# Kernel tuning notes

Measured on AMD Instinct MI355X. Metric: run time of the kernel, lower is better.

Reference implementation:

```python
import jax, jax.numpy as jnp
import numpy as np

B, N, D, K, L, H, DFF = 2048, 64, 256, 32, 2, 8, 1024
TEMP = 10.0
EPS = 1e-10


def _ln(x, g, b):
    m = jnp.mean(x, -1, keepdims=True)
    v = jnp.mean((x - m) ** 2, -1, keepdims=True)
    return (x - m) * jax.lax.rsqrt(v + 1e-5) * g + b


def _mha(x, Wqkv, bqkv, Wo, bo):
    b, n, d = x.shape
    dh = d // H
    qkv = x @ Wqkv.T + bqkv                      # [b,n,3d]
    q, k, v = jnp.split(qkv, 3, axis=-1)
    q = q.reshape(b, n, H, dh)
    k = k.reshape(b, n, H, dh)
    v = v.reshape(b, n, H, dh)
    att = jnp.einsum('bqhd,bkhd->bhqk', q, k) / np.float32(np.sqrt(dh))
    att = jax.nn.softmax(att, axis=-1)
    o = jnp.einsum('bhqk,bkhd->bqhd', att, v).reshape(b, n, d)
    return o @ Wo.T + bo


def _encoder(x, Wqkv, bqkv, Wo, bo, ln1_g, ln1_b, ln2_g, ln2_b, W1, b1, W2, b2):
    # torch TransformerEncoder, norm_first=False (post-LN), dropout=0
    for l in range(L):
        x = _ln(x + _mha(x, Wqkv[l], bqkv[l], Wo[l], bo[l]), ln1_g[l], ln1_b[l])
        h = jax.nn.relu(x @ W1[l].T + b1[l]) @ W2[l].T + b2[l]
        x = _ln(x + h, ln2_g[l], ln2_b[l])
    return x


def _cluster_probs_from_emb(emb, mus):
    # ||x - tanh(mu)||^2 via expansion to avoid the [B,N,K,D] intermediate
    mt = jnp.tanh(mus)                                       # [K,D]
    d2 = (jnp.sum(emb ** 2, -1)[..., None]
          - 2.0 * jnp.einsum('bnd,kd->bnk', emb, mt)
          + jnp.sum(mt ** 2, -1))                            # [B,N,K]
    e = jnp.exp(-d2 / TEMP)
    return e / jnp.sum(e, -1, keepdims=True)


def _forward(input_series, init_logits, transition_logits,
             Wqkv, bqkv, Wo, bo, ln1_g, ln1_b, ln2_g, ln2_b,
             W1, b1, W2, b2, mus):
    prob_pi = jax.nn.softmax(init_logits, axis=0)            # [K]
    prob_A = jax.nn.softmax(transition_logits, axis=1)       # [K,K]
    emb_all = _encoder(input_series, Wqkv, bqkv, Wo, bo,
                       ln1_g, ln1_b, ln2_g, ln2_b, W1, b1, W2, b2)
    logits_all = _cluster_probs_from_emb(emb_all, mus)       # [B,N,K]

    log_emit = jnp.log(logits_all + EPS)                     # [B,N,K]
    lt0 = jax.nn.softmax(jnp.log(prob_pi + EPS)[None, :] + log_emit[:, 0], axis=1)

    def step(lt, le):
        lt = jax.nn.softmax(jnp.log(lt @ prob_A + EPS) + le, axis=1)
        return lt, lt

    _, rest = jax.lax.scan(step, lt0, jnp.swapaxes(log_emit[:, 1:], 0, 1))
    cluster_probs = jnp.concatenate([lt0[:, None], jnp.swapaxes(rest, 0, 1)], axis=1)
    entropy_loss = -jnp.mean(jnp.sum(cluster_probs * jnp.log(cluster_probs + EPS), -1))
    return cluster_probs, emb_all, prob_pi, prob_A, entropy_loss


def setup_inputs() -> dict:
    key = jax.random.key(0)
    ks = jax.random.split(key, 10)
    s = jnp.float32(0.02)
    return {
        'input_series': jax.random.normal(ks[0], (B, N, D), jnp.float32),
        'init_logits': jax.random.normal(ks[1], (K,), jnp.float32),
        'transition_logits': jax.random.normal(ks[2], (K, K), jnp.float32),
        'Wqkv': jax.random.normal(ks[3], (L, 3 * D, D), jnp.float32) * s,
        'bqkv': jnp.zeros((L, 3 * D), jnp.float32),
        'Wo': jax.random.normal(ks[4], (L, D, D), jnp.float32) * s,
        'bo': jnp.zeros((L, D), jnp.float32),
        'ln1_g': jnp.ones((L, D), jnp.float32),
        'ln1_b': jnp.zeros((L, D), jnp.float32),
        'ln2_g': jnp.ones((L, D), jnp.float32),
        'ln2_b': jnp.zeros((L, D), jnp.float32),
        'W1': jax.random.normal(ks[5], (L, DFF, D), jnp.float32) * s,
        'b1': jnp.zeros((L, DFF), jnp.float32),
        'W2': jax.random.normal(ks[6], (L, D, DFF), jnp.float32) * s,
        'b2': jnp.zeros((L, D), jnp.float32),
        'mus': jax.random.normal(ks[7], (K, D), jnp.float32),
    }


def reference(input_series, init_logits, transition_logits, Wqkv, bqkv, Wo, bo,
              ln1_g, ln1_b, ln2_g, ln2_b, W1, b1, W2, b2, mus):
    return _forward(input_series, init_logits, transition_logits, Wqkv, bqkv,
                    Wo, bo, ln1_g, ln1_b, ln2_g, ln2_b, W1, b1, W2, b2, mus)
```

## Files before the change

kernel.cpp:

```cpp
#include <hip/hip_runtime.h>

#define BB   2048
#define NNX  64
#define DD   256
#define KKC  32
#define LLN  2
#define HHN  8
#define DHH  32
#define DFFN 1024
#define BNT  (BB*NNX)

typedef short s16x8 __attribute__((ext_vector_type(8)));
typedef float f32x4 __attribute__((ext_vector_type(4)));

#define GLOAD_LDS16(gp, lp) __builtin_amdgcn_global_load_lds( \
    (const __attribute__((address_space(1))) void*)(gp),      \
    (__attribute__((address_space(3))) void*)(lp), 16, 0, 0)

#define WAITVM4() asm volatile("s_waitcnt vmcnt(4)" ::: "memory")
#define WAITVM0() asm volatile("s_waitcnt vmcnt(0)" ::: "memory")
#define SBAR() __builtin_amdgcn_s_barrier()

__device__ __forceinline__ unsigned short f2bf(float f) {
  unsigned int u = __float_as_uint(f);
  u += 0x7fffu + ((u >> 16) & 1u);
  return (unsigned short)(u >> 16);
}
__device__ __forceinline__ float bf2f(unsigned short u) {
  return __uint_as_float(((unsigned int)u) << 16);
}

__global__ __launch_bounds__(256) void cvt_kernel(const float4* __restrict__ src,
                                                  ushort4* __restrict__ dst, int n4) {
  int i = blockIdx.x * 256 + threadIdx.x;
  int st = gridDim.x * 256;
  for (; i < n4; i += st) {
    float4 v = src[i];
    ushort4 o;
    o.x = f2bf(v.x); o.y = f2bf(v.y); o.z = f2bf(v.z); o.w = f2bf(v.w);
    dst[i] = o;
  }
}

__global__ void mt_kernel(const float* __restrict__ mus, float* __restrict__ mtT,
                          float* __restrict__ mtn) {
  int k = threadIdx.x;
  if (k < 32) {
    float acc = 0.f;
    for (int d = 0; d < 256; d++) {
      float t = tanhf(mus[k * 256 + d]);
      mtT[d * 32 + k] = t;
      acc += t * t;
    }
    mtn[k] = acc;
  }
}

__global__ void piA_kernel(const float* __restrict__ il, const float* __restrict__ tl,
                           float* __restrict__ d_pi, float* __restrict__ d_A,
                           float* __restrict__ d_ent) {
  int lane = threadIdx.x;
  if (lane == 0) *d_ent = 0.f;
  if (lane < 32) {
    float v = il[lane];
    float mx = v;
    #pragma unroll
    for (int off = 16; off; off >>= 1) mx = fmaxf(mx, __shfl_xor(mx, off, 32));
    float e = expf(v - mx), sm = e;
    #pragma unroll
    for (int off = 16; off; off >>= 1) sm += __shfl_xor(sm, off, 32);
    d_pi[lane] = e / sm;
    for (int r = 0; r < 32; r++) {
      float a = tl[r * 32 + lane];
      float m2 = a;
      #pragma unroll
      for (int off = 16; off; off >>= 1) m2 = fmaxf(m2, __shfl_xor(m2, off, 32));
      float e2 = expf(a - m2), s2 = e2;
      #pragma unroll
      for (int off = 16; off; off >>= 1) s2 += __shfl_xor(s2, off, 32);
      d_A[r * 32 + lane] = e2 / s2;
    }
  }
}

template <int EPI>
__global__ __launch_bounds__(256, 4) void gemm_nt(const unsigned short* __restrict__ A,
                                                  const unsigned short* __restrict__ Bw,
                                                  const float* __restrict__ bias,
                                                  unsigned short* __restrict__ outp,
                                                  int N, int K, int nx) {
  __shared__ unsigned short lds[16384];
  const int t = threadIdx.x;
  const int bid = blockIdx.x, nwg = gridDim.x;
  const int wg = (bid & 7) * (nwg >> 3) + (bid >> 3);
  const int m0 = (wg / nx) << 7;
  const int n0 = (wg % nx) << 7;
  const int lane = t & 63, w = t >> 6;
  const int wm = w >> 1, wn = w & 1;
  const int lr = lane & 15, lk = lane >> 4;

  const int r0 = t >> 2, sg = t & 3;
  const int s0 = sg ^ ((r0 >> 1) & 3);
  const int r1 = r0 + 64;
  const int s1 = sg ^ ((r1 >> 1) & 3);
  const int aoff0 = (m0 + r0) * K + s0 * 8;
  const int aoff1 = (m0 + r1) * K + s1 * 8;
  const int boff0 = (n0 + r0) * K + s0 * 8;
  const int boff1 = (n0 + r1) * K + s1 * 8;

#define STAGE(buf, k0) do {                                    \
    char* la = (char*)lds + (buf) * 16384;                     \
    GLOAD_LDS16(A + aoff0 + (k0), la + t * 16);                \
    GLOAD_LDS16(A + aoff1 + (k0), la + 4096 + t * 16);         \
    GLOAD_LDS16(Bw + boff0 + (k0), la + 8192 + t * 16);        \
    GLOAD_LDS16(Bw + boff1 + (k0), la + 12288 + t * 16);       \
  } while (0)

  f32x4 acc[4][4];
  #pragma unroll
  for (int i = 0; i < 4; i++)
    #pragma unroll
    for (int j = 0; j < 4; j++) acc[i][j] = (f32x4)(0.f);

  const int ra = wm * 64 + lr, rb = wn * 64 + lr;
  const int sla = lk ^ ((ra >> 1) & 3), slb = lk ^ ((rb >> 1) & 3);

  const int NT = K >> 5;
  STAGE(0, 0);
  STAGE(1, 32);
  WAITVM4();
  SBAR();

  int c = 0;
  for (int kt = 0; kt < NT; kt++) {
    s16x8 af[4], bf[4];
    {
      const unsigned short* ua = lds + c * 8192;
      const unsigned short* ub = ua + 4096;
      #pragma unroll
      for (int mf = 0; mf < 4; mf++)
        af[mf] = *(const s16x8*)&ua[(ra + mf * 16) * 32 + sla * 8];
      #pragma unroll
      for (int nf = 0; nf < 4; nf++)
        bf[nf] = *(const s16x8*)&ub[(rb + nf * 16) * 32 + slb * 8];
    }
    __builtin_amdgcn_s_setprio(1);
    #pragma unroll
    for (int mf = 0; mf < 4; mf++)
      #pragma unroll
      for (int nf = 0; nf < 4; nf++)
        acc[mf][nf] = __builtin_amdgcn_mfma_f32_16x16x32_bf16(af[mf], bf[nf], acc[mf][nf], 0, 0, 0);
    __builtin_amdgcn_s_setprio(0);
    SBAR();
    if (kt < NT - 2) {
      STAGE(c, (kt + 2) << 5);
      WAITVM4();
    } else if (kt == NT - 2) {
      WAITVM0();
    }
    SBAR();
    c ^= 1;
  }
#undef STAGE

  #pragma unroll
  for (int nf = 0; nf < 4; nf++) {
    int col = n0 + wn * 64 + nf * 16 + lr;
    float bv = bias[col];
    #pragma unroll
    for (int mf = 0; mf < 4; mf++)
      #pragma unroll
      for (int r = 0; r < 4; r++) {
        int row = m0 + wm * 64 + mf * 16 + lk * 4 + r;
        float v = acc[mf][nf][r] + bv;
        if (EPI == 1) v = fmaxf(v, 0.f);
        outp[(size_t)row * N + col] = f2bf(v);
      }
  }
}

template <bool WR32>
__global__ __launch_bounds__(512) void gemm_ln(const unsigned short* __restrict__ A,
                                               const unsigned short* __restrict__ Bw,
                                               const float* __restrict__ bias,
                                               const unsigned short* __restrict__ res,
                                               const float* __restrict__ g,
                                               const float* __restrict__ bta,
                                               unsigned short* __restrict__ xb,
                                               float* __restrict__ x32,
                                               int K) {
  __shared__ unsigned short As[128 * 64];
  __shared__ unsigned short Bs[256 * 64];
  __shared__ float stats[2][128][4];
  const int t = threadIdx.x;
  const int nwg = gridDim.x;
  const int bid = blockIdx.x;
  const int wg = (bid & 7) * (nwg >> 3) + (bid >> 3);
  const int m0 = wg << 7;

  const int lane = t & 63, w = t >> 6;
  const int wm = w >> 2, wn = w & 3;
  const int lr = lane & 15, lk = lane >> 4;

  size_t aoff[2], boff[4];
  #pragma unroll
  for (int p = 0; p < 2; p++) {
    int u = p * 512 + t;
    int row = u >> 3, sp = u & 7;
    int seg = sp ^ (((row >> 2) & 1) << 1);
    aoff[p] = (size_t)(m0 + row) * K + seg * 8;
  }
  #pragma unroll
  for (int p = 0; p < 4; p++) {
    int u = p * 512 + t;
    int row = u >> 3, sp = u & 7;
    int seg = sp ^ (((row >> 2) & 1) << 1);
    boff[p] = (size_t)row * K + seg * 8;
  }

  f32x4 acc[4][4];
  #pragma unroll
  for (int i = 0; i < 4; i++)
    #pragma unroll
    for (int j = 0; j < 4; j++) acc[i][j] = (f32x4)(0.f);

  for (int k0 = 0; k0 < K; k0 += 64) {
    #pragma unroll
    for (int p = 0; p < 2; p++)
      GLOAD_LDS16(A + aoff[p] + k0, (char*)As + (p * 512 + t) * 16);
    #pragma unroll
    for (int p = 0; p < 4; p++)
      GLOAD_LDS16(Bw + boff[p] + k0, (char*)Bs + (p * 512 + t) * 16);
    __syncthreads();
    #pragma unroll
    for (int z = 0; z < 2; z++) {
      s16x8 af[4], bfr[4];
      #pragma unroll
      for (int mf = 0; mf < 4; mf++) {
        int row = wm * 64 + mf * 16 + lr;
        int cc = (z * 4 + lk) ^ (((row >> 2) & 1) << 1);
        af[mf] = *(const s16x8*)&As[row * 64 + cc * 8];
      }
      #pragma unroll
      for (int nf = 0; nf < 4; nf++) {
        int row = wn * 64 + nf * 16 + lr;
        int cc = (z * 4 + lk) ^ (((row >> 2) & 1) << 1);
        bfr[nf] = *(const s16x8*)&Bs[row * 64 + cc * 8];
      }
      #pragma unroll
      for (int mf = 0; mf < 4; mf++)
        #pragma unroll
        for (int nf = 0; nf < 4; nf++)
          acc[mf][nf] = __builtin_amdgcn_mfma_f32_16x16x32_bf16(af[mf], bfr[nf], acc[mf][nf], 0, 0, 0);
    }
    __syncthreads();
  }

  float bv[4];
  #pragma unroll
  for (int nf = 0; nf < 4; nf++) bv[nf] = bias[wn * 64 + nf * 16 + lr];

  #pragma unroll
  for (int mf = 0; mf < 4; mf++) {
    #pragma unroll
    for (int r = 0; r < 4; r++) {
      int grow = m0 + wm * 64 + mf * 16 + lk * 4 + r;
      float s = 0.f, q = 0.f;
      #pragma unroll
      for (int nf = 0; nf < 4; nf++) {
        int col = wn * 64 + nf * 16 + lr;
        float v = acc[mf][nf][r] + bv[nf] + bf2f(res[(size_t)grow * 256 + col]);
        acc[mf][nf][r] = v;
        s += v; q += v * v;
      }
      #pragma unroll
      for (int off = 1; off < 16; off <<= 1) { s += __shfl_xor(s, off); q += __shfl_xor(q, off); }
      if (lr == 0) {
        int lrow = wm * 64 + mf * 16 + lk * 4 + r;
        stats[0][lrow][wn] = s;
        stats[1][lrow][wn] = q;
      }
    }
  }
  __syncthreads();

  float gv[4], bbv[4];
  #pragma unroll
  for (int nf = 0; nf < 4; nf++) {
    int col = wn * 64 + nf * 16 + lr;
    gv[nf] = g[col]; bbv[nf] = bta[col];
  }
  #pragma unroll
  for (int mf = 0; mf < 4; mf++) {
    #pragma unroll
    for (int r = 0; r < 4; r++) {
      int lrow = wm * 64 + mf * 16 + lk * 4 + r;
      int grow = m0 + lrow;
      float s4 = stats[0][lrow][0] + stats[0][lrow][1] + stats[0][lrow][2] + stats[0][lrow][3];
      float q4 = stats[1][lrow][0] + stats[1][lrow][1] + stats[1][lrow][2] + stats[1][lrow][3];
      float mean = s4 * (1.f / 256.f);
      float var = q4 * (1.f / 256.f) - mean * mean;
      float rs = rsqrtf(var + 1e-5f);
      #pragma unroll
      for (int nf = 0; nf < 4; nf++) {
        int col = wn * 64 + nf * 16 + lr;
        float val = (acc[mf][nf][r] - mean) * rs * gv[nf] + bbv[nf];
        xb[(size_t)grow * 256 + col] = f2bf(val);
        if (WR32) x32[(size_t)grow * 256 + col] = val;
      }
    }
  }
}

__global__ __launch_bounds__(64) void attn_kernel(const unsigned short* __restrict__ qkv,
                                                  unsigned short* __restrict__ ob) {
  __shared__ unsigned short qs[64 * 32], ks[64 * 32], vs[64 * 32];
  __shared__ unsigned short ps[64 * 72];
  const int bh = blockIdx.x;
  const int b = bh >> 3, h = bh & 7;
  const int lane = threadIdx.x;
  const int lr = lane & 15, lk = lane >> 4;

  #pragma unroll
  for (int p = 0; p < 4; p++) {
    int u = lane + p * 64;
    int row = u >> 2, seg = u & 3;
    size_t gb = (size_t)(b * 64 + row) * 768 + h * 32 + seg * 8;
    GLOAD_LDS16(qkv + gb, (char*)qs + u * 16);
    GLOAD_LDS16(qkv + gb + 256, (char*)ks + u * 16);
    GLOAD_LDS16(qkv + gb + 512, (char*)vs + u * 16);
  }
  __syncthreads();

  f32x4 s[4][4];
  #pragma unroll
  for (int i = 0; i < 4; i++)
    #pragma unroll
    for (int j = 0; j < 4; j++) s[i][j] = (f32x4)(0.f);
  s16x8 aq[4], bk[4];
  #pragma unroll
  for (int mi = 0; mi < 4; mi++) aq[mi] = *(const s16x8*)&qs[(mi * 16 + lr) * 32 + lk * 8];
  #pragma unroll
  for (int nj = 0; nj < 4; nj++) bk[nj] = *(const s16x8*)&ks[(nj * 16 + lr) * 32 + lk * 8];
  #pragma unroll
  for (int mi = 0; mi < 4; mi++)
    #pragma unroll
    for (int nj = 0; nj < 4; nj++)
      s[mi][nj] = __builtin_amdgcn_mfma_f32_16x16x32_bf16(aq[mi], bk[nj], s[mi][nj], 0, 0, 0);

  const float scale = 0.17677669529663687f;
  #pragma unroll
  for (int mi = 0; mi < 4; mi++) {
    #pragma unroll
    for (int r = 0; r < 4; r++) {
      float t0 = s[mi][0][r] * scale, t1 = s[mi][1][r] * scale;
      float t2 = s[mi][2][r] * scale, t3 = s[mi][3][r] * scale;
      float mx = fmaxf(fmaxf(t0, t1), fmaxf(t2, t3));
      #pragma unroll
      for (int off = 8; off; off >>= 1) mx = fmaxf(mx, __shfl_xor(mx, off, 16));
      float e0 = expf(t0 - mx), e1 = expf(t1 - mx), e2 = expf(t2 - mx), e3 = expf(t3 - mx);
      float sm = e0 + e1 + e2 + e3;
      #pragma unroll
      for (int off = 8; off; off >>= 1) sm += __shfl_xor(sm, off, 16);
      float inv = 1.f / sm;
      int prow = mi * 16 + lk * 4 + r;
      ps[prow * 72 + lr + 0]  = f2bf(e0 * inv);
      ps[prow * 72 + lr + 16] = f2bf(e1 * inv);
      ps[prow * 72 + lr + 32] = f2bf(e2 * inv);
      ps[prow * 72 + lr + 48] = f2bf(e3 * inv);
    }
  }
  __syncthreads();

  f32x4 oacc[4][2];
  #pragma unroll
  for (int i = 0; i < 4; i++) { oacc[i][0] = (f32x4)(0.f); oacc[i][1] = (f32x4)(0.f); }
  #pragma unroll
  for (int kk = 0; kk < 2; kk++) {
    s16x8 bv[2];
    #pragma unroll
    for (int nf = 0; nf < 2; nf++) {
      s16x8 tmp;
      #pragma unroll
      for (int jj = 0; jj < 8; jj++)
        tmp[jj] = (short)vs[(kk * 32 + lk * 8 + jj) * 32 + nf * 16 + lr];
      bv[nf] = tmp;
    }
    #pragma unroll
    for (int mi = 0; mi < 4; mi++) {
      s16x8 ap = *(const s16x8*)&ps[(mi * 16 + lr) * 72 + kk * 32 + lk * 8];
      #pragma unroll
      for (int nf = 0; nf < 2; nf++)
        oacc[mi][nf] = __builtin_amdgcn_mfma_f32_16x16x32_bf16(ap, bv[nf], oacc[mi][nf], 0, 0, 0);
    }
  }
  #pragma unroll
  for (int mi = 0; mi < 4; mi++)
    #pragma unroll
    for (int nf = 0; nf < 2; nf++)
      #pragma unroll
      for (int r = 0; r < 4; r++) {
        int tok = mi * 16 + lk * 4 + r;
        int c = nf * 16 + lr;
        ob[(size_t)(b * 64 + tok) * 256 + h * 32 + c] = f2bf(oacc[mi][nf][r]);
      }
}

__global__ __launch_bounds__(256) void cluster_kernel(const float* __restrict__ x,
                                                      const float* __restrict__ mtT,
                                                      const float* __restrict__ mtn,
                                                      float* __restrict__ log_emit) {
  __shared__ float mts[8192];
  __shared__ float es[4][256];
  const int t = threadIdx.x;
  #pragma unroll
  for (int i = 0; i < 8; i++)
    ((float4*)mts)[i * 256 + t] = ((const float4*)mtT)[i * 256 + t];
  const int w = t >> 6, lane = t & 63;
  const int k = lane & 31, half = lane >> 5;
  const float mtnr = mtn[k];
  __syncthreads();
  #pragma unroll 1
  for (int it = 0; it < 8; it++) {
    size_t tok = (size_t)blockIdx.x * 32 + (size_t)w * 8 + it;
    float4 u = *((const float4*)(x + tok * 256) + lane);
    *(float4*)&es[w][lane * 4] = u;
    float e2 = u.x * u.x + u.y * u.y + u.z * u.z + u.w * u.w;
    #pragma unroll
    for (int off = 1; off < 64; off <<= 1) e2 += __shfl_xor(e2, off);
    float acc = 0.f;
    const float* ep = &es[w][half * 128];
    const float* mp = &mts[half * 128 * 32 + k];
    #pragma unroll
    for (int d = 0; d < 128; d += 4) {
      float4 ev = *(const float4*)(ep + d);
      acc += ev.x * mp[(d + 0) * 32] + ev.y * mp[(d + 1) * 32]
           + ev.z * mp[(d + 2) * 32] + ev.w * mp[(d + 3) * 32];
    }
    acc += __shfl_xor(acc, 32);
    float d2 = e2 - 2.f * acc + mtnr;
    float e = expf(-d2 * 0.1f);
    float sm = e;
    #pragma unroll
    for (int off = 16; off; off >>= 1) sm += __shfl_xor(sm, off, 32);
    if (half == 0) log_emit[tok * 32 + k] = logf(e / sm + 1e-10f);
  }
}

__global__ __launch_bounds__(256) void scan_kernel(const float* __restrict__ log_emit,
                                                   const float* __restrict__ pi,
                                                   const float* __restrict__ A,
                                                   float* __restrict__ cp,
                                                   float* __restrict__ ent) {
  const int g = threadIdx.x >> 5, j = threadIdx.x & 31;
  const int batch = blockIdx.x * 8 + g;
  float regA[32];
  #pragma unroll
  for (int i = 0; i < 32; i++) regA[i] = A[i * 32 + j];
  const float* le = log_emit + (size_t)batch * 64 * 32;
  float* cpo = cp + (size_t)batch * 64 * 32;

  float u = logf(pi[j] + 1e-10f) + le[j];
  float mx = u;
  #pragma unroll
  for (int off = 16; off; off >>= 1) mx = fmaxf(mx, __shfl_xor(mx, off, 32));
  float e = expf(u - mx), sm = e;
  #pragma unroll
  for (int off = 16; off; off >>= 1) sm += __shfl_xor(sm, off, 32);
  float p = e / sm;
  cpo[j] = p;
  float enta = p * logf(p + 1e-10f);

  for (int n = 1; n < 64; n++) {
    float tt = 0.f;
    #pragma unroll
    for (int i = 0; i < 32; i++) tt += __shfl(p, i, 32) * regA[i];
    u = logf(tt + 1e-10f) + le[n * 32 + j];
    mx = u;
    #pragma unroll
    for (int off = 16; off; off >>= 1) mx = fmaxf(mx, __shfl_xor(mx, off, 32));
    e = expf(u - mx); sm = e;
    #pragma unroll
    for (int off = 16; off; off >>= 1) sm += __shfl_xor(sm, off, 32);
    p = e / sm;
    cpo[n * 32 + j] = p;
    enta += p * logf(p + 1e-10f);
  }
  #pragma unroll
  for (int off = 16; off; off >>= 1) enta += __shfl_xor(enta, off, 32);
  if (j == 0) atomicAdd(ent, -enta * (1.f / (2048.f * 64.f)));
}

extern "C" void kernel_launch(void* const* d_in, const int* in_sizes, int n_in,
                              void* d_out, int out_size, void* d_ws, size_t ws_size,
                              hipStream_t stream) {
  const float* input = (const float*)d_in[0];
  const float* init_logits = (const float*)d_in[1];
  const float* trans = (const float*)d_in[2];
  const float* Wqkv = (const float*)d_in[3];
  const float* bqkv = (const float*)d_in[4];
  const float* Wo = (const float*)d_in[5];
  const float* bo = (const float*)d_in[6];
  const float* ln1g = (const float*)d_in[7];
  const float* ln1b = (const float*)d_in[8];
  const float* ln2g = (const float*)d_in[9];
  const float* ln2b = (const float*)d_in[10];
  const float* W1 = (const float*)d_in[11];
  const float* b1 = (const float*)d_in[12];
  const float* W2 = (const float*)d_in[13];
  const float* b2 = (const float*)d_in[14];
  const float* mus = (const float*)d_in[15];

  float* out = (float*)d_out;
  float* cp = out;
  float* x = out + 4194304;
  float* d_pi = out + 37748736;
  float* d_A = out + 37748768;
  float* d_ent = out + 37749792;

  char* ws = (char*)d_ws;
  unsigned short* qkv = (unsigned short*)ws;
  unsigned short* hb = (unsigned short*)ws;
  float* log_emit = (float*)ws;
  unsigned short* ob = (unsigned short*)(ws + 268435456ull);
  unsigned short* xb = (unsigned short*)(ws + 335544320ull);
  unsigned short* wq_b = (unsigned short*)(ws + 402653184ull);
  unsigned short* wo_b = (unsigned short*)(ws + 402653184ull + 786432ull);
  unsigned short* w1_b = (unsigned short*)(ws + 402653184ull + 1048576ull);
  unsigned short* w2_b = (unsigned short*)(ws + 402653184ull + 2097152ull);
  float* mtT = (float*)(ws + 402653184ull + 3145728ull);
  float* mtn = (float*)(ws + 402653184ull + 3178496ull);

  cvt_kernel<<<2048, 256, 0, stream>>>((const float4*)input, (ushort4*)xb, BNT * 256 / 4);
  cvt_kernel<<<256, 256, 0, stream>>>((const float4*)Wqkv, (ushort4*)wq_b, LLN * 768 * 256 / 4);
  cvt_kernel<<<256, 256, 0, stream>>>((const float4*)Wo, (ushort4*)wo_b, LLN * 256 * 256 / 4);
  cvt_kernel<<<256, 256, 0, stream>>>((const float4*)W1, (ushort4*)w1_b, LLN * 1024 * 256 / 4);
  cvt_kernel<<<256, 256, 0, stream>>>((const float4*)W2, (ushort4*)w2_b, LLN * 256 * 1024 / 4);
  mt_kernel<<<1, 64, 0, stream>>>(mus, mtT, mtn);
  piA_kernel<<<1, 64, 0, stream>>>(init_logits, trans, d_pi, d_A, d_ent);

  for (int l = 0; l < 2; l++) {
    gemm_nt<0><<<6144, 256, 0, stream>>>(xb, wq_b + l * 196608, bqkv + l * 768,
                                         qkv, 768, 256, 6);
    attn_kernel<<<16384, 64, 0, stream>>>(qkv, ob);
    gemm_ln<false><<<1024, 512, 0, stream>>>(ob, wo_b + l * 65536, bo + l * 256,
                                             xb, ln1g + l * 256, ln1b + l * 256,
                                             xb, nullptr, 256);
    gemm_nt<1><<<8192, 256, 0, stream>>>(xb, w1_b + l * 262144, b1 + l * 1024,
                                         hb, 1024, 256, 8);
    if (l == LLN - 1)
      gemm_ln<true><<<1024, 512, 0, stream>>>(hb, w2_b + l * 262144, b2 + l * 256,
                                              xb, ln2g + l * 256, ln2b + l * 256,
                                              xb, x, 1024);
    else
      gemm_ln<false><<<1024, 512, 0, stream>>>(hb, w2_b + l * 262144, b2 + l * 256,
                                               xb, ln2g + l * 256, ln2b + l * 256,
                                               xb, nullptr, 1024);
  }

  cluster_kernel<<<4096, 256, 0, stream>>>(x, mtT, mtn, log_emit);
  scan_kernel<<<256, 256, 0, stream>>>(log_emit, d_pi, d_A, cp, d_ent);
}
```

Measured before the change: 1.247 ms.

## Double-buffer gemm_ln K-loop with BK=32 stages and async prefetch

Rewrites the gemm_ln main loop from a single-buffered BK=64 load-then-compute scheme into a two-stage ring with BK=32 tiles. The next tile's global-to-LDS loads are issued while MFMAs run on the current buffer, with vmcnt waits and barriers in place of full syncthreads. It also raises MFMA wave priority, reuses the tile LDS for LN stats, and adds an occupancy hint. The intent is to hide global load latency behind compute, at the cost of more barriers per K step and a new XOR swizzle that must stay correct.

```diff
diff --git a/kernel.cpp b/kernel.cpp
--- a/kernel.cpp
+++ b/kernel.cpp
@@ -18,6 +18,7 @@
     (__attribute__((address_space(3))) void*)(lp), 16, 0, 0)
 
 #define WAITVM4() asm volatile("s_waitcnt vmcnt(4)" ::: "memory")
+#define WAITVM3() asm volatile("s_waitcnt vmcnt(3)" ::: "memory")
 #define WAITVM0() asm volatile("s_waitcnt vmcnt(0)" ::: "memory")
 #define SBAR() __builtin_amdgcn_s_barrier()
 
@@ -180,21 +181,19 @@
 }
 
 template <bool WR32>
-__global__ __launch_bounds__(512) void gemm_ln(const unsigned short* __restrict__ A,
-                                               const unsigned short* __restrict__ Bw,
-                                               const float* __restrict__ bias,
-                                               const unsigned short* __restrict__ res,
-                                               const float* __restrict__ g,
-                                               const float* __restrict__ bta,
-                                               unsigned short* __restrict__ xb,
-                                               float* __restrict__ x32,
-                                               int K) {
-  __shared__ unsigned short As[128 * 64];
-  __shared__ unsigned short Bs[256 * 64];
-  __shared__ float stats[2][128][4];
+__global__ __launch_bounds__(512, 4) void gemm_ln(const unsigned short* __restrict__ A,
+                                                  const unsigned short* __restrict__ Bw,
+                                                  const float* __restrict__ bias,
+                                                  const unsigned short* __restrict__ res,
+                                                  const float* __restrict__ g,
+                                                  const float* __restrict__ bta,
+                                                  unsigned short* __restrict__ xb,
+                                                  float* __restrict__ x32,
+                                                  int K) {
+  __shared__ unsigned short lds[24576];
+  float* stats = (float*)lds;
   const int t = threadIdx.x;
-  const int nwg = gridDim.x;
-  const int bid = blockIdx.x;
+  const int bid = blockIdx.x, nwg = gridDim.x;
   const int wg = (bid & 7) * (nwg >> 3) + (bid >> 3);
   const int m0 = wg << 7;
 
@@ -202,21 +201,18 @@
   const int wm = w >> 2, wn = w & 3;
   const int lr = lane & 15, lk = lane >> 4;
 
-  size_t aoff[2], boff[4];
-  #pragma unroll
-  for (int p = 0; p < 2; p++) {
-    int u = p * 512 + t;
-    int row = u >> 3, sp = u & 7;
-    int seg = sp ^ (((row >> 2) & 1) << 1);
-    aoff[p] = (size_t)(m0 + row) * K + seg * 8;
-  }
-  #pragma unroll
-  for (int p = 0; p < 4; p++) {
-    int u = p * 512 + t;
-    int row = u >> 3, sp = u & 7;
-    int seg = sp ^ (((row >> 2) & 1) << 1);
-    boff[p] = (size_t)row * K + seg * 8;
-  }
+  const int r0 = t >> 2, sg = t & 3;
+  const int s0 = sg ^ ((r0 >> 1) & 3);
+  const int aoff = (m0 + r0) * K + s0 * 8;
+  const int boff0 = r0 * K + s0 * 8;
+  const int boff1 = (128 + r0) * K + s0 * 8;
+
+#define STAGE(buf, k0) do {                                    \
+    char* la = (char*)lds + (buf) * 24576;                     \
+    GLOAD_LDS16(A + aoff + (k0),   la + t * 16);               \
+    GLOAD_LDS16(Bw + boff0 + (k0), la + 8192 + t * 16);        \
+    GLOAD_LDS16(Bw + boff1 + (k0), la + 16384 + t * 16);       \
+  } while (0)
 
   f32x4 acc[4][4];
   #pragma unroll
@@ -224,38 +220,48 @@
     #pragma unroll
     for (int j = 0; j < 4; j++) acc[i][j] = (f32x4)(0.f);
 
-  for (int k0 = 0; k0 < K; k0 += 64) {
-    #pragma unroll
-    for (int p = 0; p < 2; p++)
-      GLOAD_LDS16(A + aoff[p] + k0, (char*)As + (p * 512 + t) * 16);
-    #pragma unroll
-    for (int p = 0; p < 4; p++)
-      GLOAD_LDS16(Bw + boff[p] + k0, (char*)Bs + (p * 512 + t) * 16);
-    __syncthreads();
-    #pragma unroll
-    for (int z = 0; z < 2; z++) {
-      s16x8 af[4], bfr[4];
-      #pragma unroll
-      for (int mf = 0; mf < 4; mf++) {
-        int row = wm * 64 + mf * 16 + lr;
-        int cc = (z * 4 + lk) ^ (((row >> 2) & 1) << 1);
-        af[mf] = *(const s16x8*)&As[row * 64 + cc * 8];
-      }
-      #pragma unroll
-      for (int nf = 0; nf < 4; nf++) {
-        int row = wn * 64 + nf * 16 + lr;
-        int cc = (z * 4 + lk) ^ (((row >> 2) & 1) << 1);
-        bfr[nf] = *(const s16x8*)&Bs[row * 64 + cc * 8];
-      }
+  const int ra = wm * 64 + lr, rb = wn * 64 + lr;
+  const int sla = lk ^ ((ra >> 1) & 3), slb = lk ^ ((rb >> 1) & 3);
+
+  const int NT = K >> 5;
+  STAGE(0, 0);
+  STAGE(1, 32);
+  WAITVM3();
+  SBAR();
+
+  int c = 0;
+  for (int kt = 0; kt < NT; kt++) {
+    s16x8 af[4], bf[4];
+    {
+      const unsigned short* ua = lds + c * 12288;
+      const unsigned short* ub = ua + 4096;
       #pragma unroll
       for (int mf = 0; mf < 4; mf++)
-        #pragma unroll
-        for (int nf = 0; nf < 4; nf++)
-          acc[mf][nf] = __builtin_amdgcn_mfma_f32_16x16x32_bf16(af[mf], bfr[nf], acc[mf][nf], 0, 0, 0);
-    }
-    __syncthreads();
-  }
-
+        af[mf] = *(const s16x8*)&ua[(ra + mf * 16) * 32 + sla * 8];
+      #pragma unroll
+      for (int nf = 0; nf < 4; nf++)
+        bf[nf] = *(const s16x8*)&ub[(rb + nf * 16) * 32 + slb * 8];
+    }
+    __builtin_amdgcn_s_setprio(1);
+    #pragma unroll
+    for (int mf = 0; mf < 4; mf++)
+      #pragma unroll
+      for (int nf = 0; nf < 4; nf++)
+        acc[mf][nf] = __builtin_amdgcn_mfma_f32_16x16x32_bf16(af[mf], bf[nf], acc[mf][nf], 0, 0, 0);
+    __builtin_amdgcn_s_setprio(0);
+    SBAR();
+    if (kt < NT - 2) {
+      STAGE(c, (kt + 2) << 5);
+      WAITVM3();
+    } else if (kt == NT - 2) {
+      WAITVM0();
+    }
+    SBAR();
+    c ^= 1;
+  }
+#undef STAGE
+
+  __syncthreads();
   float bv[4];
   #pragma unroll
   for (int nf = 0; nf < 4; nf++) bv[nf] = bias[wn * 64 + nf * 16 + lr];
@@ -264,7 +270,8 @@
   for (int mf = 0; mf < 4; mf++) {
     #pragma unroll
     for (int r = 0; r < 4; r++) {
-      int grow = m0 + wm * 64 + mf * 16 + lk * 4 + r;
+      int lrow = wm * 64 + mf * 16 + lk * 4 + r;
+      int grow = m0 + lrow;
       float s = 0.f, q = 0.f;
       #pragma unroll
       for (int nf = 0; nf < 4; nf++) {
@@ -275,11 +282,7 @@
       }
       #pragma unroll
       for (int off = 1; off < 16; off <<= 1) { s += __shfl_xor(s, off); q += __shfl_xor(q, off); }
-      if (lr == 0) {
-        int lrow = wm * 64 + mf * 16 + lk * 4 + r;
-        stats[0][lrow][wn] = s;
-        stats[1][lrow][wn] = q;
-      }
+      if (lr == 0) { stats[lrow * 4 + wn] = s; stats[512 + lrow * 4 + wn] = q; }
     }
   }
   __syncthreads();
@@ -296,8 +299,9 @@
     for (int r = 0; r < 4; r++) {
       int lrow = wm * 64 + mf * 16 + lk * 4 + r;
       int grow = m0 + lrow;
-      float s4 = stats[0][lrow][0] + stats[0][lrow][1] + stats[0][lrow][2] + stats[0][lrow][3];
-      float q4 = stats[1][lrow][0] + stats[1][lrow][1] + stats[1][lrow][2] + stats[1][lrow][3];
+      float s4 = stats[lrow * 4 + 0] + stats[lrow * 4 + 1] + stats[lrow * 4 + 2] + stats[lrow * 4 + 3];
+      float q4 = stats[512 + lrow * 4 + 0] + stats[512 + lrow * 4 + 1]
+               + stats[512 + lrow * 4 + 2] + stats[512 + lrow * 4 + 3];
       float mean = s4 * (1.f / 256.f);
       float var = q4 * (1.f / 256.f) - mean * mean;
       float rs = rsqrtf(var + 1e-5f);
```

After: 1.289 ms. +3.4%, slower.
